# Performance work log

Measured on AMD Instinct MI355X. Metric: run time of the kernel, lower is better.

Reference implementation:

```python
import jax, jax.numpy as jnp
import numpy as np

B_, K_, D_, L_, N_, R_ = 4, 4, 96, 2048, 16, 6
C_ = R_ + 2 * N_  # 38


def setup_inputs() -> dict:
    key = jax.random.key(0)
    ks = jax.random.split(key, 6)
    scale = 0.05  # keep projections in a realistic range (like 1/sqrt(fan_in) init)
    return {
        "xs": jax.random.normal(ks[0], (B_, K_, D_, L_), dtype=jnp.float32),
        "A_logs": jax.random.uniform(ks[1], (K_ * D_, N_), dtype=jnp.float32),
        "Ds": jax.random.normal(ks[2], (K_ * D_,), dtype=jnp.float32),
        "dt_projs_weight": jax.random.normal(ks[3], (K_, D_, R_), dtype=jnp.float32) * scale,
        "dt_projs_bias": jax.random.normal(ks[4], (K_, D_), dtype=jnp.float32) * scale,
        "x_proj_weight": jax.random.normal(ks[5], (K_, C_, D_), dtype=jnp.float32) * scale,
    }


def reference(xs, A_logs, Ds, dt_projs_weight, dt_projs_bias, x_proj_weight):
    B, K, D, L = xs.shape
    N = A_logs.shape[1]
    R = dt_projs_weight.shape[2]

    xs = xs.astype(jnp.float32)  # force_fp32=True

    # project x -> (delta, B, C):  [B,K,C,L]
    x_dbl = jnp.einsum("bkdl,kcd->bkcl", xs, x_proj_weight)
    dts, Bs, Cs = x_dbl[:, :, :R], x_dbl[:, :, R:R + N], x_dbl[:, :, R + N:]
    # dt low-rank -> per-channel delta: [B,K,D,L]
    dts = jnp.einsum("bkrl,kdr->bkdl", dts, dt_projs_weight)

    A = -jnp.exp(A_logs.astype(jnp.float32)).reshape(K, D, N)  # [K,D,N]
    Dskd = Ds.astype(jnp.float32).reshape(K, D)

    # delta_softplus with delta_bias
    delta = jax.nn.softplus(dts + dt_projs_bias.astype(jnp.float32)[None, :, :, None])

    # discretization: deltaA [B,K,D,L,N], deltaB_u [B,K,D,L,N]
    dA = jnp.exp(delta[..., None] * A[None, :, :, None, :])
    dBu = jnp.einsum("bkdl,bknl,bkdl->bkdln", delta, Bs, xs)

    # linear recurrence h_t = dA_t * h_{t-1} + dBu_t via parallel associative scan over L
    def combine(e1, e2):
        a1, b1 = e1
        a2, b2 = e2
        return a1 * a2, a2 * b1 + b2

    _, hs = jax.lax.associative_scan(combine, (dA, dBu), axis=3)  # hs: [B,K,D,L,N]

    # y_t = C_t . h_t + D * x_t
    y = jnp.einsum("bkdln,bknl->bkdl", hs, Cs) + Dskd[None, :, :, None] * xs
    return y.astype(jnp.float32)  # [B,K,D,L]
```

## Files before the change

kernel.cpp:

```cpp
#include <hip/hip_runtime.h>
#include <hip/hip_fp16.h>
#include <math.h>

#define B_ 4
#define K_ 4
#define D_ 96
#define L_ 2048
#define N_ 16
#define R_ 6
#define C_ 38

__device__ __forceinline__ float softplus_f(float x) {
    return fmaxf(x, 0.f) + __logf(1.f + __expf(-fabsf(x)));
}

#if __has_builtin(__builtin_amdgcn_exp2f)
__device__ __forceinline__ float exp2_fast(float x) { return __builtin_amdgcn_exp2f(x); }
#else
__device__ __forceinline__ float exp2_fast(float x) { return __expf(0.6931471805599453f * x); }
#endif

__device__ __forceinline__ float h2f(const uint4& v, int e) {
    return __half2float(((const __half*)&v)[e]);
}


__global__ __launch_bounds__(256) void proj_kernel(
    const float* __restrict__ xs, const float* __restrict__ xpw,
    uint4* __restrict__ BCc, float* __restrict__ dts_ws)
{
    __shared__ float sWt[D_][8];
    const int bk = blockIdx.x;
    const int k = bk & 3;
    const int cg = blockIdx.z;
    const int tid = threadIdx.x;

    int c0, nr;
    if (cg < 4)       { c0 = R_ + cg * 8; nr = 8; }
    else if (cg == 4) { c0 = 0;           nr = 4; }
    else              { c0 = 4;           nr = 2; }

    for (int i = tid; i < 8 * D_; i += 256) {
        const int r = i / D_, dd = i % D_;
        sWt[dd][r] = (r < nr) ? xpw[(k * C_ + c0 + r) * D_ + dd] : 0.f;
    }
    __syncthreads();

    const int l = blockIdx.y * 256 + tid;
    const float* Xl = xs + (size_t)bk * D_ * L_ + l;

    float acc[8];
#pragma unroll
    for (int r = 0; r < 8; ++r) acc[r] = 0.f;

#pragma unroll
    for (int d = 0; d < D_; ++d) {
        const float xv = Xl[d * L_];
        float4 w0 = *(const float4*)&sWt[d][0];
        float4 w1 = *(const float4*)&sWt[d][4];
        acc[0] = fmaf(w0.x, xv, acc[0]); acc[1] = fmaf(w0.y, xv, acc[1]);
        acc[2] = fmaf(w0.z, xv, acc[2]); acc[3] = fmaf(w0.w, xv, acc[3]);
        acc[4] = fmaf(w1.x, xv, acc[4]); acc[5] = fmaf(w1.y, xv, acc[5]);
        acc[6] = fmaf(w1.z, xv, acc[6]); acc[7] = fmaf(w1.w, xv, acc[7]);
    }

    if (cg < 4) {
        const int i8 = l & 7, t8 = l >> 3;
        union { __half h[8]; uint4 v; } p;
#pragma unroll
        for (int e = 0; e < 8; ++e) p.h[e] = __float2half(acc[e]);
        BCc[(((size_t)bk * 8 + i8) * 4 + cg) * 256 + t8] = p.v;
    } else {
        const int rbase = (cg == 4) ? 0 : 4;
        const int rcnt = (cg == 4) ? 4 : 2;
        for (int r = 0; r < rcnt; ++r)
            dts_ws[((size_t)bk * R_ + rbase + r) * L_ + l] = acc[r];
    }
}

__global__ __launch_bounds__(512) void scan_kernel(
    const float* __restrict__ xs, const float* __restrict__ A_logs,
    const float* __restrict__ Ds, const float* __restrict__ dtw,
    const float* __restrict__ dtb, const float* __restrict__ dts_ws,
    const uint4* __restrict__ BCc, float* __restrict__ out)
{
    __shared__ float sAw[8][8];
    __shared__ float sBw[8][8];
    __shared__ float sy[256][9];

    const int bkd = blockIdx.x;
    const int d = bkd % D_;
    const int bk = bkd / D_;
    const int k = bk & 3;
    const int kd = k * D_ + d;
    const int tid = threadIdx.x;
    const int g = tid >> 8;
    const int t = tid & 255;
    const int lane = tid & 63;
    const int gw = tid >> 6;

    const uint4* BC = BCc + (size_t)bk * 8 * 4 * 256;
    const int jB = g, jC = 2 + g;

    const float4* xv4 = (const float4*)(xs + (size_t)bkd * L_);
    const float4 xa = xv4[t * 2], xb = xv4[t * 2 + 1];
    float x[8] = {xa.x, xa.y, xa.z, xa.w, xb.x, xb.y, xb.z, xb.w};

    float del[8];
    const float bias = dtb[kd];
#pragma unroll
    for (int j = 0; j < 8; ++j) del[j] = bias;
    const float* w2 = dtw + (size_t)kd * R_;
    const float4* dts4 = (const float4*)(dts_ws + (size_t)bk * R_ * L_);
#pragma unroll
    for (int r = 0; r < R_; ++r) {
        const float wr = w2[r];
        const float4 t0 = dts4[r * (L_ / 4) + t * 2];
        const float4 t1 = dts4[r * (L_ / 4) + t * 2 + 1];
        del[0] = fmaf(wr, t0.x, del[0]); del[1] = fmaf(wr, t0.y, del[1]);
        del[2] = fmaf(wr, t0.z, del[2]); del[3] = fmaf(wr, t0.w, del[3]);
        del[4] = fmaf(wr, t1.x, del[4]); del[5] = fmaf(wr, t1.y, del[5]);
        del[6] = fmaf(wr, t1.z, del[6]); del[7] = fmaf(wr, t1.w, del[7]);
    }
#pragma unroll
    for (int j = 0; j < 8; ++j) del[j] = softplus_f(del[j]);

    float A2[8];
    const float* Ap = A_logs + (size_t)kd * N_ + g * 8;
#pragma unroll
    for (int n = 0; n < 8; ++n) A2[n] = -__expf(Ap[n]) * 1.44269504f;
    const float Dval = Ds[kd];

    float a[8], b[8];
#pragma unroll
    for (int n = 0; n < 8; ++n) { a[n] = 1.f; b[n] = 0.f; }
#pragma unroll
    for (int i = 0; i < 8; ++i) {
        const uint4 cB = BC[(i * 4 + jB) * 256 + t];
        const float dl = del[i];
        const float dx = dl * x[i];
#pragma unroll
        for (int n = 0; n < 8; ++n) {
            const float dA = exp2_fast(dl * A2[n]);
            b[n] = fmaf(dA, b[n], dx * h2f(cB, n));
            a[n] *= dA;
        }
    }

#pragma unroll
    for (int off = 1; off < 64; off <<= 1) {
#pragma unroll
        for (int n = 0; n < 8; ++n) {
            const float pa = __shfl_up(a[n], off, 64);
            const float pb = __shfl_up(b[n], off, 64);
            if (lane >= off) {
                b[n] = fmaf(a[n], pb, b[n]);
                a[n] *= pa;
            }
        }
    }
    if (lane == 63) {
#pragma unroll
        for (int n = 0; n < 8; ++n) { sAw[gw][n] = a[n]; sBw[gw][n] = b[n]; }
    }
    __syncthreads();

    float h[8];
#pragma unroll
    for (int n = 0; n < 8; ++n) {
        float ae = __shfl_up(a[n], 1, 64);
        float be = __shfl_up(b[n], 1, 64);
        if (lane == 0) { ae = 1.f; be = 0.f; }
        float wb = 0.f;
        for (int w = g * 4; w < gw; ++w) wb = fmaf(sAw[w][n], wb, sBw[w][n]);
        h[n] = fmaf(ae, wb, be);
    }

    float yv[8];
#pragma unroll
    for (int j = 0; j < 8; ++j) yv[j] = (g == 0) ? Dval * x[j] : 0.f;
#pragma unroll
    for (int i = 0; i < 8; ++i) {
        const uint4 cB = BC[(i * 4 + jB) * 256 + t];
        const uint4 cC = BC[(i * 4 + jC) * 256 + t];
        const float dl = del[i];
        const float dx = dl * x[i];
        float y = yv[i];
#pragma unroll
        for (int n = 0; n < 8; ++n) {
            const float dA = exp2_fast(dl * A2[n]);
            h[n] = fmaf(dA, h[n], dx * h2f(cB, n));
            y = fmaf(h[n], h2f(cC, n), y);
        }
        yv[i] = y;
    }

    if (g == 1) {
#pragma unroll
        for (int j = 0; j < 8; ++j) sy[t][j] = yv[j];
    }
    __syncthreads();
    if (g == 0) {
#pragma unroll
        for (int j = 0; j < 8; ++j) yv[j] += sy[t][j];
        float4* ov = (float4*)(out + (size_t)bkd * L_);
        ov[t * 2]     = make_float4(yv[0], yv[1], yv[2], yv[3]);
        ov[t * 2 + 1] = make_float4(yv[4], yv[5], yv[6], yv[7]);
    }
}

extern "C" void kernel_launch(void* const* d_in, const int* in_sizes, int n_in,
                              void* d_out, int out_size, void* d_ws, size_t ws_size,
                              hipStream_t stream) {
    const float* xs = (const float*)d_in[0];
    const float* A_logs = (const float*)d_in[1];
    const float* Ds = (const float*)d_in[2];
    const float* dtw = (const float*)d_in[3];
    const float* dtb = (const float*)d_in[4];
    const float* xpw = (const float*)d_in[5];
    float* out = (float*)d_out;

    uint4* BCc = (uint4*)d_ws;
    float* dts_ws = (float*)(BCc + (size_t)B_ * K_ * 8 * 4 * 256);

    proj_kernel<<<dim3(B_ * K_, 8, 6), 256, 0, stream>>>(xs, xpw, BCc, dts_ws);
    scan_kernel<<<B_ * K_ * D_, 512, 0, stream>>>(
        xs, A_logs, Ds, dtw, dtb, dts_ws, BCc, out);
}
```

Baseline: 123.0 us.

## Eliminate second scan pass by decomposing output into local and carry-in terms

Instead of recomputing the recurrence in a second pass after the cross-thread prefix, each thread now computes local y contributions during the first pass and stores C_n*cumulative-a weights for each step. The final output adds w[i][n]*h0[n] for the carry-in state, removing a second round of exp2 evaluations and B/C loads. This adds 64 registers for the w array, which may increase register pressure and lower occupancy at 512 threads per block.

```diff
diff --git a/kernel.cpp b/kernel.cpp
--- a/kernel.cpp
+++ b/kernel.cpp
@@ -131,20 +131,33 @@
     for (int n = 0; n < 8; ++n) A2[n] = -__expf(Ap[n]) * 1.44269504f;
     const float Dval = Ds[kd];
 
-    float a[8], b[8];
+    float dlx[8], yv[8];
+#pragma unroll
+    for (int j = 0; j < 8; ++j) {
+        dlx[j] = del[j] * x[j];
+        yv[j] = (g == 0) ? Dval * x[j] : 0.f;
+    }
+
+    float a[8], b[8], w[8][8];
 #pragma unroll
     for (int n = 0; n < 8; ++n) { a[n] = 1.f; b[n] = 0.f; }
 #pragma unroll
     for (int i = 0; i < 8; ++i) {
         const uint4 cB = BC[(i * 4 + jB) * 256 + t];
+        const uint4 cC = BC[(i * 4 + jC) * 256 + t];
         const float dl = del[i];
-        const float dx = dl * x[i];
+        const float dx = dlx[i];
+        float zi = 0.f;
 #pragma unroll
         for (int n = 0; n < 8; ++n) {
             const float dA = exp2_fast(dl * A2[n]);
             b[n] = fmaf(dA, b[n], dx * h2f(cB, n));
             a[n] *= dA;
+            const float Cn = h2f(cC, n);
+            zi = fmaf(Cn, b[n], zi);
+            w[i][n] = Cn * a[n];
         }
+        yv[i] += zi;
     }
 
 #pragma unroll
@@ -165,34 +178,22 @@
     }
     __syncthreads();
 
-    float h[8];
+    float h0[8];
 #pragma unroll
     for (int n = 0; n < 8; ++n) {
         float ae = __shfl_up(a[n], 1, 64);
         float be = __shfl_up(b[n], 1, 64);
         if (lane == 0) { ae = 1.f; be = 0.f; }
         float wb = 0.f;
-        for (int w = g * 4; w < gw; ++w) wb = fmaf(sAw[w][n], wb, sBw[w][n]);
-        h[n] = fmaf(ae, wb, be);
-    }
-
-    float yv[8];
-#pragma unroll
-    for (int j = 0; j < 8; ++j) yv[j] = (g == 0) ? Dval * x[j] : 0.f;
+        for (int wv = g * 4; wv < gw; ++wv) wb = fmaf(sAw[wv][n], wb, sBw[wv][n]);
+        h0[n] = fmaf(ae, wb, be);
+    }
+
 #pragma unroll
     for (int i = 0; i < 8; ++i) {
-        const uint4 cB = BC[(i * 4 + jB) * 256 + t];
-        const uint4 cC = BC[(i * 4 + jC) * 256 + t];
-        const float dl = del[i];
-        const float dx = dl * x[i];
-        float y = yv[i];
-#pragma unroll
-        for (int n = 0; n < 8; ++n) {
-            const float dA = exp2_fast(dl * A2[n]);
-            h[n] = fmaf(dA, h[n], dx * h2f(cB, n));
-            y = fmaf(h[n], h2f(cC, n), y);
-        }
-        yv[i] = y;
+#pragma unroll
+        for (int n = 0; n < 8; ++n)
+            yv[i] = fmaf(w[i][n], h0[n], yv[i]);
     }
 
     if (g == 1) {
```

Measured after the change: 123.7 us. No clear change (+0.5%).
